# Kernel tuning notes

Hardware: AMD Instinct MI355X
Metric: run time of the kernel (lower is better)

## Reference

```python
import jax, jax.numpy as jnp
import numpy as np
import math

# ---- model dims (match init_kwargs) ----
D_MODEL = 1024
EXPAND = 2
HEADDIM = 64
D_STATE = 128
NGROUPS = 1
CHUNK = 64
A_FLOOR = 1e-4
D_INNER = EXPAND * D_MODEL            # 2048
NHEADS = D_INNER // HEADDIM           # 32
ROPE_DIM = D_STATE // 2               # rope_fraction=0.5 -> rotate half the state dims
NROPE = ROPE_DIM // 2                 # 32 rotation angles
D_IN_PROJ = D_INNER + 2 * D_STATE * NGROUPS + 3 * NHEADS + NROPE  # 2432
B, L = 2, 2048
EPS = 1e-5


def setup_inputs() -> dict:
    key = jax.random.key(0)
    ks = jax.random.split(key, 5)
    u = jax.random.normal(ks[0], (B, L, D_MODEL), dtype=jnp.float32)
    W_in = jax.random.normal(ks[1], (D_IN_PROJ, D_MODEL), dtype=jnp.float32) * 0.02
    W_out = jax.random.normal(ks[2], (D_MODEL, D_INNER), dtype=jnp.float32) * 0.02
    # dt_bias init as in the torch module
    dt_min, dt_max, dt_floor = 1e-3, 1e-1, 1e-4
    dt = jnp.exp(jax.random.uniform(ks[3], (NHEADS,)) * (math.log(dt_max) - math.log(dt_min)) + math.log(dt_min))
    dt = jnp.maximum(dt, dt_floor)
    dt_bias = dt + jnp.log(-jnp.expm1(-dt))
    B_bias = jnp.ones((NHEADS, D_STATE), dtype=jnp.float32)
    C_bias = jnp.ones((NHEADS, D_STATE), dtype=jnp.float32)
    Bnorm_w = jnp.ones((D_STATE,), dtype=jnp.float32)
    Cnorm_w = jnp.ones((D_STATE,), dtype=jnp.float32)
    D = jnp.ones((NHEADS,), dtype=jnp.float32)
    return {"u": u, "W_in": W_in, "dt_bias": dt_bias, "B_bias": B_bias, "C_bias": C_bias,
            "Bnorm_w": Bnorm_w, "Cnorm_w": Cnorm_w, "D": D, "W_out": W_out}


def _rmsnorm(v, w):
    return v * jax.lax.rsqrt(jnp.mean(v * v, axis=-1, keepdims=True) + EPS) * w


def _rope(v, cos, sin):
    # rotate first 2*NROPE dims of last axis (pairs (i, i+NROPE)); rest untouched
    x1 = v[..., :NROPE]
    x2 = v[..., NROPE:2 * NROPE]
    rest = v[..., 2 * NROPE:]
    return jnp.concatenate([x1 * cos - x2 * sin, x1 * sin + x2 * cos, rest], axis=-1)


def _forward(u, W_in, dt_bias, B_bias, C_bias, Bnorm_w, Cnorm_w, D, W_out):
    b, l, _ = u.shape
    proj = jnp.einsum('bld,ed->ble', u, W_in)
    idx = np.cumsum([D_INNER, D_STATE * NGROUPS, D_STATE * NGROUPS, NHEADS, NHEADS, NHEADS])[:-1].tolist()
    x, Braw, Craw, dd_dt, dd_A, trap_angles = jnp.split(proj, [D_INNER, D_INNER + D_STATE, D_INNER + 2 * D_STATE,
                                                                D_INNER + 2 * D_STATE + NHEADS,
                                                                D_INNER + 2 * D_STATE + 2 * NHEADS], axis=-1)
    trap = trap_angles[..., :NHEADS]
    angles = trap_angles[..., NHEADS:NHEADS + NROPE]
    x = x.reshape(b, l, NHEADS, HEADDIM)

    # discretization scalars per (b,l,h)
    A = -jax.nn.softplus(dd_A)
    A = jnp.minimum(A, -A_FLOOR)
    DT = jax.nn.softplus(dd_dt + dt_bias)
    la = A * DT                      # log of per-step decay (negative)
    a = jnp.exp(la)

    # RMSNorm on B/C (ngroups=1), broadcast to heads, add per-head bias
    Bn = _rmsnorm(Braw, Bnorm_w)[:, :, None, :] + B_bias   # (b,l,h,n)
    Cn = _rmsnorm(Craw, Cnorm_w)[:, :, None, :] + C_bias

    # inline RoPE: cumulative angle Theta_t = cumsum(angles_t * dt_t)
    theta = angles[:, :, None, :] * DT[..., None]           # (b,l,h,r)
    Theta = jnp.cumsum(theta, axis=1)
    cosT, sinT = jnp.cos(Theta), jnp.sin(Theta)
    Bn = _rope(Bn, cosT, sinT)
    Cn = _rope(Cn, cosT, sinT)

    # trapezoidal integration weights: dt*(lam*B_t x_t + (1-lam)*exp(A dt)*B_{t-1} x_{t-1})
    lam = jax.nn.sigmoid(trap)
    w1 = DT * lam                    # current-token weight  (b,l,h)
    w2 = DT * (1.0 - lam) * a        # previous-token weight (includes decay)
    Bp = jnp.pad(Bn, ((0, 0), (1, 0), (0, 0), (0, 0)))[:, :-1]
    xp = jnp.pad(x, ((0, 0), (1, 0), (0, 0), (0, 0)))[:, :-1]

    # ---- chunked selective scan ----
    nc = l // CHUNK
    ck = lambda t: t.reshape(b, nc, CHUNK, *t.shape[2:])
    xc, xpc, Bc, Bpc, Cc = ck(x), ck(xp), ck(Bn), ck(Bp), ck(Cn)
    lac, w1c, w2c = ck(la), ck(w1), ck(w2)
    Acum = jnp.cumsum(lac, axis=2)                           # (b,z,t,h)

    mask = jnp.tril(jnp.ones((CHUNK, CHUNK), dtype=u.dtype))
    decay = jnp.exp(Acum[:, :, :, None, :] - Acum[:, :, None, :, :]) * mask[None, None, :, :, None]  # (b,z,t,s,h)

    CB1 = jnp.einsum('bzthn,bzshn->bztsh', Cc, Bc)
    CB2 = jnp.einsum('bzthn,bzshn->bztsh', Cc, Bpc)
    M1 = decay * CB1 * w1c[:, :, None, :, :]
    M2 = decay * CB2 * w2c[:, :, None, :, :]
    Yintra = jnp.einsum('bztsh,bzshp->bzthp', M1, xc) + jnp.einsum('bztsh,bzshp->bzthp', M2, xpc)

    # contribution of each chunk to its end-of-chunk state
    r = jnp.exp(Acum[:, :, -1:, :] - Acum)                   # (b,z,t,h)
    U = (jnp.einsum('bzsh,bzshn,bzshp->bzhpn', r * w1c, Bc, xc)
         + jnp.einsum('bzsh,bzshn,bzshp->bzhpn', r * w2c, Bpc, xpc))
    cd = jnp.exp(Acum[:, :, -1, :])                          # whole-chunk decay (b,z,h)

    def step(h, inp):
        U_, c_ = inp
        return c_[..., None, None] * h + U_, h               # emit state at chunk start
    h0 = jnp.zeros((b, NHEADS, HEADDIM, D_STATE), dtype=u.dtype)
    _, states = jax.lax.scan(step, h0, (jnp.moveaxis(U, 1, 0), jnp.moveaxis(cd, 1, 0)))  # (z,b,h,p,n)

    Ystate = jnp.einsum('bzthn,bzth,zbhpn->bzthp', Cc, jnp.exp(Acum), states)
    y = (Yintra + Ystate).reshape(b, l, NHEADS, HEADDIM) + x * D[None, None, :, None]
    y = y.reshape(b, l, D_INNER)
    return jnp.einsum('bli,oi->blo', y, W_out)


def reference(u, W_in, dt_bias, B_bias, C_bias, Bnorm_w, Cnorm_w, D, W_out):
    return _forward(u, W_in, dt_bias, B_bias, C_bias, Bnorm_w, Cnorm_w, D, W_out)
```

## Files before the change

kernel.cpp:

```cpp
#include <hip/hip_runtime.h>
#include <hip/hip_bf16.h>
#include <math.h>

typedef unsigned short u16;
typedef __attribute__((ext_vector_type(8))) short s16x8;
typedef __attribute__((ext_vector_type(4))) float f32x4;

#define BB 2
#define LL 2048
#define DMODEL 1024
#define DI 2048
#define NH 32
#define HD 64
#define DS 128
#define NR 32
#define CH 64
#define NC 32
#define DIP 2432
#define NTOK (BB*LL)
#define PAW 384
#define CVW 264

__device__ __forceinline__ float bf2f(u16 u){ union{unsigned i; float f;} c; c.i=((unsigned)u)<<16; return c.f; }
__device__ __forceinline__ u16 f2bf(float f){ __hip_bfloat16 h=__float2bfloat16(f); return *reinterpret_cast<u16*>(&h); }
__device__ __forceinline__ float softplusf(float x){ return fmaxf(x,0.f) + log1pf(expf(-fabsf(x))); }

__device__ __forceinline__ void gl_lds16(const void* g, void* l){
  __builtin_amdgcn_global_load_lds((const __attribute__((address_space(1))) void*)g,
                                   (__attribute__((address_space(3))) void*)l, 16, 0, 0);
}

__device__ __forceinline__ s16x8 ldswz(const u16* base, int r, int kunit){
  return *(const s16x8*)&base[r*128 + ((kunit ^ (r&7))<<3)];
}
__device__ __forceinline__ s16x8 ldswz64(const u16* base, int r, int kunit){
  return *(const s16x8*)&base[r*64 + ((kunit ^ (r&7))<<3)];
}
__device__ __forceinline__ float ldswz64_s(const u16* base, int r, int n){
  return bf2f(base[r*64 + (((n>>3) ^ (r&7))<<3) + (n&7)]);
}
__device__ __forceinline__ s16x8 ld72(const u16* base, int r, int kelem){
  return *(const s16x8*)&base[r*72 + kelem];
}

#define CQ1 ((NTOK*DMODEL)/4)
#define CQ2 ((DIP*DMODEL)/4)
#define CQ3 ((DMODEL*DI)/4)
__global__ __launch_bounds__(256) void k_cast3(const float* __restrict__ u, const float* __restrict__ Wi,
                                               const float* __restrict__ Wo,
                                               u16* __restrict__ ub, u16* __restrict__ wib,
                                               u16* __restrict__ wob){
  int i = blockIdx.x*256 + threadIdx.x;
  const float* src; u16* dst; int q;
  if (i < CQ1){ src = u; dst = ub; q = i; }
  else if (i < CQ1+CQ2){ src = Wi; dst = wib; q = i - CQ1; }
  else if (i < CQ1+CQ2+CQ3){ src = Wo; dst = wob; q = i - CQ1 - CQ2; }
  else return;
  float4 v = *(const float4*)&src[(size_t)q*4];
  ushort4 o; o.x=f2bf(v.x); o.y=f2bf(v.y); o.z=f2bf(v.z); o.w=f2bf(v.w);
  *(ushort4*)&dst[(size_t)q*4] = o;
}

__global__ __launch_bounds__(512) void k_gemm_in(const u16* __restrict__ A,
                                                 const u16* __restrict__ Bm,
                                                 float* __restrict__ pAux,
                                                 u16* __restrict__ Xtg){
  __shared__ u16 lA[128*64];
  __shared__ u16 lB[128*64];
  int tid = threadIdx.x;
  int l = tid & 63, w = tid >> 6;
  int nwg = gridDim.x*gridDim.y;
  int flat = blockIdx.y*gridDim.x + blockIdx.x;
  int cpx = nwg >> 3;
  int swz = (flat & 7)*cpx + (flat >> 3);
  int bx = swz % gridDim.x, by = swz / gridDim.x;
  int bm = by*128, bn = bx*128;
  int wr = w >> 2, wc = w & 3;
  const f32x4 vzero = {0.f,0.f,0.f,0.f};
  f32x4 acc[4][2];
  #pragma unroll
  for (int i=0;i<4;i++)
    #pragma unroll
    for (int j=0;j<2;j++) acc[i][j] = vzero;

  for (int kt=0; kt<DMODEL; kt+=64){
    __syncthreads();
    #pragma unroll
    for (int cc=0; cc<2; cc++){
      int s = w*2 + cc;
      int uu = s*64 + l;
      int r = uu >> 3, jl = uu & 7;
      int j = jl ^ (r & 7);
      gl_lds16(A  + (size_t)(bm+r)*DMODEL + kt + j*8, &lA[s*512]);
      gl_lds16(Bm + (size_t)(bn+r)*DMODEL + kt + j*8, &lB[s*512]);
    }
    __syncthreads();
    #pragma unroll
    for (int ks=0; ks<2; ks++){
      s16x8 af[4], bf[2];
      #pragma unroll
      for (int i=0;i<4;i++){
        int row = wr*64 + i*16 + (l&15);
        int j = ks*4 + (l>>4);
        af[i] = *(const s16x8*)&lA[row*64 + (j^(row&7))*8];
      }
      #pragma unroll
      for (int i=0;i<2;i++){
        int row = wc*32 + i*16 + (l&15);
        int j = ks*4 + (l>>4);
        bf[i] = *(const s16x8*)&lB[row*64 + (j^(row&7))*8];
      }
      #pragma unroll
      for (int i=0;i<4;i++)
        #pragma unroll
        for (int jj=0;jj<2;jj++)
          acc[i][jj] = __builtin_amdgcn_mfma_f32_16x16x32_bf16(af[i], bf[jj], acc[i][jj], 0,0,0);
    }
  }
  int col0 = bn + wc*32 + (l&15);
  int row0 = bm + wr*64 + (l>>4)*4;
  if (bn < DI){
    int h = (bn + wc*32) >> 6;
    int pbase = (wc & 1)*32 + (l&15);
    int b = bm >> 11;
    #pragma unroll
    for (int i=0;i<4;i++){
      int lbase = (bm & (LL-1)) + wr*64 + (l>>4)*4 + i*16;
      #pragma unroll
      for (int jj=0;jj<2;jj++){
        int p = pbase + jj*16;
        ushort4 o;
        o.x = f2bf(acc[i][jj][0]); o.y = f2bf(acc[i][jj][1]);
        o.z = f2bf(acc[i][jj][2]); o.w = f2bf(acc[i][jj][3]);
        *(ushort4*)&Xtg[((size_t)(b*NH + h)*HD + p)*LL + lbase] = o;
      }
    }
  } else {
    #pragma unroll
    for (int i=0;i<4;i++)
      #pragma unroll
      for (int jj=0;jj<2;jj++)
        #pragma unroll
        for (int q=0;q<4;q++)
          pAux[(size_t)(row0 + i*16 + q)*PAW + col0 + jj*16 - DI] = acc[i][jj][q];
  }
}

__global__ __launch_bounds__(256) void k_prep(const float* __restrict__ pAux,
                                              const float* __restrict__ dt_bias,
                                              const float* __restrict__ Bnw,
                                              const float* __restrict__ Cnw,
                                              float* __restrict__ Bnr, float* __restrict__ Cnr,
                                              float* __restrict__ DTg, float* __restrict__ lag,
                                              float* __restrict__ w1g, float* __restrict__ w2g){
  int tid = threadIdx.x;
  int r = tid >> 7, t = tid & 127;
  int row = blockIdx.x*2 + r;
  const float* pr = pAux + (size_t)row*PAW;
  float bv = pr[t], cv = pr[128+t];
  float sb = bv*bv, sc = cv*cv;
  for (int o=32;o;o>>=1){ sb += __shfl_down(sb,o); sc += __shfl_down(sc,o); }
  __shared__ float red[8];
  if ((tid&63)==0){ red[(tid>>6)*2]=sb; red[(tid>>6)*2+1]=sc; }
  __syncthreads();
  float ssb = red[r*4]+red[r*4+2], ssc = red[r*4+1]+red[r*4+3];
  float rb = rsqrtf(ssb/DS + 1e-5f), rc = rsqrtf(ssc/DS + 1e-5f);
  Bnr[(size_t)row*DS+t] = bv*rb*Bnw[t];
  Cnr[(size_t)row*DS+t] = cv*rc*Cnw[t];
  if (t < NH){
    int h = t;
    float Av = -softplusf(pr[288+h]); Av = fminf(Av, -1e-4f);
    float DT = softplusf(pr[256+h] + dt_bias[h]);
    float la = Av*DT;
    float lam = 1.f/(1.f+expf(-pr[320+h]));
    DTg[row*NH+h] = DT;
    lag[row*NH+h] = la;
    w1g[row*NH+h] = DT*lam;
    w2g[row*NH+h] = DT*(1.f-lam)*expf(la);
  }
}

__global__ __launch_bounds__(64) void k_theta_part(const float* __restrict__ pAux, const float* __restrict__ DTg,
                                                   float* __restrict__ Spart){
  int blk = blockIdx.x*2 + (threadIdx.x>>5);
  int j = threadIdx.x & 31;
  int h = blk % NH; int z = (blk/NH)%NC; int b = blk/(NH*NC);
  float acc = 0.f;
  for (int i=0;i<CH;i++){
    int row = b*LL + z*CH + i;
    acc += DTg[row*NH+h] * pAux[(size_t)row*PAW + 352 + j];
  }
  Spart[(size_t)blk*NR + j] = acc;
}

__global__ void k_theta_scan(float* __restrict__ Spart){
  int idx = blockIdx.x*blockDim.x + threadIdx.x;
  int j = idx % NR; int h = (idx/NR)%NH; int b = idx/(NR*NH);
  float acc = 0.f;
  for (int z=0;z<NC;z++){
    size_t o = (size_t)((b*NC+z)*NH + h)*NR + j;
    float t = Spart[o]; Spart[o] = acc; acc += t;
  }
}

__global__ __launch_bounds__(256) void k_acum(const float* __restrict__ lag,
                                              const float* __restrict__ w1g,
                                              const float* __restrict__ w2g,
                                              float* __restrict__ CV,
                                              float* __restrict__ Acumg,
                                              float* __restrict__ cdg){
  int blk = blockIdx.x*4 + (threadIdx.x>>6);
  int l = threadIdx.x & 63;
  int h = blk & 31, z = (blk>>5)&31, b = blk>>10;
  int row = b*LL + z*CH + l;
  float la = lag[row*NH+h], w1 = w1g[row*NH+h], w2 = w2g[row*NH+h];
  float a = la;
  #pragma unroll
  for (int o=1;o<64;o<<=1){ float t = __shfl_up(a,o); a += (l>=o) ? t : 0.f; }
  float Acm = __shfl(a, 31);
  float Alast = __shfl(a, 63);
  float eA = expf(a - Acm);
  float emA = expf(Acm - a);
  float rfac = expf(Alast - a);
  float rw1 = rfac*w1, rw2 = rfac*w2;
  float rw1p = __shfl_up(rw1, 1);
  float* cv = CV + (size_t)blk*CVW;
  cv[l] = eA;
  cv[64 + l] = emA*w1;
  cv[128 + l] = emA*w2;
  cv[192 + l] = (l>0 ? rw1p : 0.f) + rw2;
  if (l == 63){ cv[192+64] = rw1; cdg[blk] = expf(Alast); }
  Acumg[(size_t)blk*CH + l] = a;
}

__global__ __launch_bounds__(256) void k_rope2(const float* __restrict__ Bnr,
                                               const float* __restrict__ Cnr,
                                               const float* __restrict__ pAux,
                                               const float* __restrict__ DTg,
                                               const float* __restrict__ Spart,
                                               const float* __restrict__ B_bias,
                                               const float* __restrict__ C_bias,
                                               u16* __restrict__ Bn, u16* __restrict__ Cn){
  __shared__ float thS[64][33];
  int blk = blockIdx.x; int h = blk&31, z=(blk>>5)&31, b=blk>>10;
  int l0 = z*CH; int tid = threadIdx.x;
  int l = tid & 63, w = tid >> 6;
  {
    int row = b*LL + l0 + l;
    float dt = DTg[row*NH + h];
    int j0 = w*8;
    float4 a0 = *(const float4*)&pAux[(size_t)row*PAW + 352 + j0];
    float4 a1 = *(const float4*)&pAux[(size_t)row*PAW + 352 + j0 + 4];
    float v[8] = {dt*a0.x, dt*a0.y, dt*a0.z, dt*a0.w, dt*a1.x, dt*a1.y, dt*a1.z, dt*a1.w};
    #pragma unroll
    for (int e=0;e<8;e++){
      float s = v[e];
      #pragma unroll
      for (int o=1;o<64;o<<=1){ float t = __shfl_up(s,o); s += (l>=o) ? t : 0.f; }
      thS[l][j0+e] = s + Spart[(size_t)blk*NR + j0 + e];
    }
  }
  __syncthreads();
  const float* bb = B_bias + h*DS;
  const float* cb = C_bias + h*DS;
  #pragma unroll
  for (int it=0; it<8; it++){
    int idx = it*256 + tid;
    int r = idx>>5, j = idx&31;
    int row = b*LL + l0 + r;
    const float* br = Bnr + (size_t)row*DS;
    const float* cr = Cnr + (size_t)row*DS;
    float th = thS[r][j];
    float cs = cosf(th), sn = sinf(th);
    float b0 = br[j]    + bb[j];
    float b1 = br[j+32] + bb[j+32];
    float b2 = br[j+64] + bb[j+64];
    float b3 = br[j+96] + bb[j+96];
    float c0 = cr[j]    + cb[j];
    float c1 = cr[j+32] + cb[j+32];
    float c2 = cr[j+64] + cb[j+64];
    float c3 = cr[j+96] + cb[j+96];
    float obA = b0*cs - b1*sn, obB = b0*sn + b1*cs;
    float ocA = c0*cs - c1*sn, ocB = c0*sn + c1*cs;
    u16* bnp = Bn + ((size_t)row*NH + h)*DS;
    u16* cnp = Cn + ((size_t)row*NH + h)*DS;
    bnp[j]    = f2bf(obA); bnp[j+32] = f2bf(obB);
    bnp[j+64] = f2bf(b2);  bnp[j+96] = f2bf(b3);
    cnp[j]    = f2bf(ocA); cnp[j+32] = f2bf(ocB);
    cnp[j+64] = f2bf(c2);  cnp[j+96] = f2bf(c3);
  }
}

__global__ __launch_bounds__(512) void k_chunk_a(
    const u16* __restrict__ Xtg, const u16* __restrict__ Bn,
    const u16* __restrict__ Cn,
    const float* __restrict__ CV, const float* __restrict__ Dgl,
    u16* __restrict__ Yb, u16* __restrict__ Ugb){
  __shared__ u16 BsBT[65*128];
  __shared__ u16 CsMc[64*128];
  __shared__ u16 Xt64[64*64];
  __shared__ u16 Bp[128], Xp[64];
  __shared__ float cvS[260];
  __shared__ float mc0s[64];
  int blk = blockIdx.x;
  int h = blk&31, z=(blk>>5)&31, b=blk>>10;
  int l0 = z*CH;
  int tid = threadIdx.x; int l = tid&63, w = tid>>6;
  int wA = w >> 1, wB = w & 1;
  size_t bh = (size_t)(b*NH + h);

  if (tid < 128){
    u16 v = 0;
    if (z > 0) v = Bn[((size_t)(b*LL+l0-1)*NH + h)*DS + tid];
    BsBT[tid] = v; Bp[tid] = v;
  } else if (tid < 192){
    int p = tid - 128;
    u16 v = 0;
    if (z > 0) v = Xtg[(bh*HD + p)*LL + l0 - 1];
    Xp[p] = v;
  }
  if (tid < 257) cvS[tid] = CV[(size_t)blk*CVW + tid];
  #pragma unroll
  for (int cc=0; cc<2; cc++){
    int c = w*2 + cc;
    { int r = 1 + 4*c + (l>>4);
      gl_lds16(Bn + ((size_t)(b*LL+l0+r-1)*NH+h)*DS + (((l&15)^(r&7))<<3), &BsBT[(1+4*c)*128]); }
    { int r = 4*c + (l>>4);
      gl_lds16(Cn + ((size_t)(b*LL+l0+r)*NH+h)*DS + (((l&15)^(r&7))<<3), &CsMc[4*c*128]); }
  }
  {
    int uu = w*64 + l; int r = uu>>3, jl = uu&7, j = jl^(r&7);
    gl_lds16(Xtg + (bh*HD + r)*LL + l0 + j*8, &Xt64[w*512]);
  }
  __syncthreads();

  const f32x4 vzero = {0.f,0.f,0.f,0.f};
  f32x4 acb[2];
  #pragma unroll
  for (int j=0;j<2;j++) acb[j] = vzero;
  #pragma unroll
  for (int ks=0; ks<4; ks++){
    s16x8 af = ldswz(CsMc, 16*wA + (l&15), ks*4 + (l>>4));
    #pragma unroll
    for (int j=0;j<2;j++){
      s16x8 bfr = ldswz(BsBT, 1 + 16*(wB*2+j) + (l&15), ks*4 + (l>>4));
      acb[j] = __builtin_amdgcn_mfma_f32_16x16x32_bf16(af, bfr, acb[j], 0,0,0);
    }
  }
  {
    int t = tid>>3, part = tid&7;
    float s = 0.f;
    #pragma unroll
    for (int uu=0; uu<2; uu++){
      int u = part*2 + uu;
      s16x8 cr = *(const s16x8*)&CsMc[t*128 + ((u^(t&7))<<3)];
      s16x8 br = *(const s16x8*)&BsBT[u<<3];
      #pragma unroll
      for (int e=0;e<8;e++) s += bf2f(cr[e])*bf2f(br[e]);
    }
    s += __shfl_xor(s, 1); s += __shfl_xor(s, 2); s += __shfl_xor(s, 4);
    if (part == 0) mc0s[t] = s * cvS[t] * cvS[128];
  }
  __syncthreads();

  u16 tv[16];
  #pragma unroll
  for (int it=0; it<16; it++){
    int i = it*512 + tid;
    int n = i & 127, k = i >> 7;
    int r = k + 1;
    tv[it] = BsBT[r*128 + ((((n>>3) ^ (r&7))<<3) | (n&7))];
  }
  #pragma unroll
  for (int j=0;j<2;j++){
    #pragma unroll
    for (int q=0;q<4;q++){
      int t = 16*wA + (l>>4)*4 + q;
      int k = 16*(wB*2+j) + (l&15);
      int sp = k + 1;
      float g = 0.f;
      if (sp <= t+1) g += cvS[63+sp];
      if (sp <= t)   g += cvS[128+sp];
      g *= cvS[t];
      CsMc[t*72 + k] = f2bf(acb[j][q] * g);
    }
  }
  __syncthreads();

  #pragma unroll
  for (int it=0; it<16; it++){
    int i = it*512 + tid;
    int n = i & 127, k = i >> 7;
    float v = bf2f(tv[it]) * cvS[192 + k + 1];
    BsBT[n*64 + ((((k>>3) ^ (n&7))<<3) | (k&7))] = f2bf(v);
  }
  __syncthreads();

  f32x4 ay[2];
  #pragma unroll
  for (int j=0;j<2;j++) ay[j] = vzero;
  #pragma unroll
  for (int ks=0; ks<2; ks++){
    s16x8 af = ld72(CsMc, 16*wA + (l&15), ks*32 + (l>>4)*8);
    #pragma unroll
    for (int j=0;j<2;j++){
      s16x8 bfr = ldswz64(Xt64, 16*(wB*2+j) + (l&15), ks*4 + (l>>4));
      ay[j] = __builtin_amdgcn_mfma_f32_16x16x32_bf16(af, bfr, ay[j], 0,0,0);
    }
  }
  {
    float Dh = Dgl[h];
    #pragma unroll
    for (int j=0;j<2;j++){
      #pragma unroll
      for (int q=0;q<4;q++){
        int t = 16*wA + (l>>4)*4 + q;
        int p = 16*(wB*2+j) + (l&15);
        float xval = ldswz64_s(Xt64, p, t);
        float yv = ay[j][q] + mc0s[t]*bf2f(Xp[p]) + Dh*xval;
        Yb[((size_t)(b*LL + l0 + t))*DI + h*HD + p] = f2bf(yv);
      }
    }
  }

  f32x4 au[4];
  #pragma unroll
  for (int j=0;j<4;j++) au[j] = vzero;
  #pragma unroll
  for (int ks=0; ks<2; ks++){
    s16x8 af = ldswz64(Xt64, 16*wA + (l&15), ks*4 + (l>>4));
    #pragma unroll
    for (int j=0;j<4;j++){
      s16x8 bfr = ldswz64(BsBT, 16*(wB*4+j) + (l&15), ks*4 + (l>>4));
      au[j] = __builtin_amdgcn_mfma_f32_16x16x32_bf16(af, bfr, au[j], 0,0,0);
    }
  }
  {
    float vw0 = cvS[192];
    #pragma unroll
    for (int j=0;j<4;j++){
      #pragma unroll
      for (int q=0;q<4;q++){
        int p = 16*wA + (l>>4)*4 + q;
        int n = 16*(wB*4+j) + (l&15);
        float uv = au[j][q] + vw0*bf2f(Xp[p])*bf2f(Bp[n]);
        Ugb[(size_t)blk*(HD*DS) + p*DS + n] = f2bf(uv);
      }
    }
  }
}

__global__ __launch_bounds__(256) void k_scan(u16* __restrict__ Ugb, const float* __restrict__ cdg){
  int idx = blockIdx.x*256 + threadIdx.x;
  int pn8 = (idx & 1023)*8;
  int h  = (idx >> 10) & 31;
  int b  = idx >> 15;
  float hs[8];
  #pragma unroll
  for (int e=0;e<8;e++) hs[e] = 0.f;
  for (int z=0;z<NC;z++){
    size_t o = ((size_t)((b*NC+z)*NH) + h)*(HD*DS) + pn8;
    s16x8 v = *(s16x8*)&Ugb[o];
    float cd = cdg[(b*NC+z)*NH + h];
    s16x8 wv;
    #pragma unroll
    for (int e=0;e<8;e++){
      float tmp = bf2f((u16)v[e]);
      wv[e] = (short)f2bf(hs[e]);
      hs[e] = cd*hs[e] + tmp;
    }
    *(s16x8*)&Ugb[o] = wv;
  }
}

__global__ __launch_bounds__(512) void k_state(
    const u16* __restrict__ Cn, const u16* __restrict__ Ugb,
    const float* __restrict__ Acumg, u16* __restrict__ Yb){
  __shared__ u16 Cs[64*128];
  __shared__ u16 Sb[64*128];
  __shared__ float eAs[64];
  int blk = blockIdx.x;
  int h = blk & 31, z = (blk>>5)&31, b = blk>>10;
  int l0 = z*CH;
  int tid = threadIdx.x;
  int l = tid & 63, w = tid >> 6;
  int wA = w >> 1, wB = w & 1;

  if (tid < 64) eAs[tid] = expf(Acumg[(size_t)blk*CH + tid]);
  #pragma unroll
  for (int cc=0; cc<2; cc++){
    int c = w*2 + cc;
    int r = 4*c + (l>>4);
    gl_lds16(Cn + ((size_t)(b*LL + l0 + r)*NH + h)*DS + (((l&15)^(r&7))<<3), &Cs[4*c*128]);
    gl_lds16(Ugb + (size_t)blk*(HD*DS) + (size_t)r*DS + (((l&15)^(r&7))<<3), &Sb[4*c*128]);
  }
  __syncthreads();

  f32x4 as[2];
  const f32x4 vzero = {0.f,0.f,0.f,0.f};
  #pragma unroll
  for (int j=0;j<2;j++) as[j] = vzero;
  #pragma unroll
  for (int ks=0; ks<4; ks++){
    s16x8 af = ldswz(Cs, 16*wA + (l&15), ks*4 + (l>>4));
    #pragma unroll
    for (int j=0;j<2;j++){
      s16x8 bfr = ldswz(Sb, 16*(wB*2+j) + (l&15), ks*4 + (l>>4));
      as[j] = __builtin_amdgcn_mfma_f32_16x16x32_bf16(af, bfr, as[j], 0,0,0);
    }
  }
  #pragma unroll
  for (int j=0;j<2;j++){
    #pragma unroll
    for (int q=0;q<4;q++){
      int t = 16*wA + (l>>4)*4 + q;
      int p = 16*(wB*2+j) + (l&15);
      size_t idx = ((size_t)(b*LL + l0 + t))*DI + h*HD + p;
      Yb[idx] = f2bf(bf2f(Yb[idx]) + eAs[t]*as[j][q]);
    }
  }
}

template<int N, int K>
__global__ __launch_bounds__(512) void k_mfma_nt64(const u16* __restrict__ A,
                                                   const u16* __restrict__ Bm,
                                                   float* __restrict__ C){
  __shared__ u16 lA[128*64];
  __shared__ u16 lB[64*64];
  int tid = threadIdx.x;
  int l = tid & 63, w = tid >> 6;
  int nwg = gridDim.x*gridDim.y;
  int flat = blockIdx.y*gridDim.x + blockIdx.x;
  int cpx = nwg >> 3;
  int swz = (flat & 7)*cpx + (flat >> 3);
  int bx = swz % gridDim.x, by = swz / gridDim.x;
  int bm = by*128, bn = bx*64;
  int wr = w >> 1, wc = w & 1;
  const f32x4 vzero = {0.f,0.f,0.f,0.f};
  f32x4 acc[2][2];
  #pragma unroll
  for (int i=0;i<2;i++)
    #pragma unroll
    for (int j=0;j<2;j++) acc[i][j] = vzero;

  for (int kt=0; kt<K; kt+=64){
    __syncthreads();
    #pragma unroll
    for (int cc=0; cc<2; cc++){
      int s = w*2 + cc;
      int uu = s*64 + l;
      int r = uu >> 3, jl = uu & 7;
      int j = jl ^ (r & 7);
      gl_lds16(A + (size_t)(bm+r)*K + kt + j*8, &lA[s*512]);
    }
    {
      int uu = w*64 + l;
      int r = uu >> 3, jl = uu & 7;
      int j = jl ^ (r & 7);
      gl_lds16(Bm + (size_t)(bn+r)*K + kt + j*8, &lB[w*512]);
    }
    __syncthreads();
    #pragma unroll
    for (int ks=0; ks<2; ks++){
      s16x8 af[2], bf[2];
      #pragma unroll
      for (int i=0;i<2;i++){
        int row = wr*32 + i*16 + (l&15);
        int j = ks*4 + (l>>4);
        af[i] = *(const s16x8*)&lA[row*64 + (j^(row&7))*8];
      }
      #pragma unroll
      for (int i=0;i<2;i++){
        int row = wc*32 + i*16 + (l&15);
        int j = ks*4 + (l>>4);
        bf[i] = *(const s16x8*)&lB[row*64 + (j^(row&7))*8];
      }
      #pragma unroll
      for (int i=0;i<2;i++)
        #pragma unroll
        for (int jj=0;jj<2;jj++)
          acc[i][jj] = __builtin_amdgcn_mfma_f32_16x16x32_bf16(af[i], bf[jj], acc[i][jj], 0,0,0);
    }
  }
  int col0 = bn + wc*32 + (l&15);
  int row0 = bm + wr*32 + (l>>4)*4;
  #pragma unroll
  for (int i=0;i<2;i++)
    #pragma unroll
    for (int jj=0;jj<2;jj++)
      #pragma unroll
      for (int q=0;q<4;q++)
        C[(size_t)(row0 + i*16 + q)*N + col0 + jj*16] = acc[i][jj][q];
}

constexpr size_t OFF_PAUX  = 0;
constexpr size_t OFF_XTG   = 6291456;
constexpr size_t OFF_BNR   = 23068672;
constexpr size_t OFF_CNR   = 25165824;
constexpr size_t OFF_DT    = 27262976;
constexpr size_t OFF_LA    = 27787264;
constexpr size_t OFF_W1    = 28311552;
constexpr size_t OFF_W2    = 28835840;
constexpr size_t OFF_SPART = 29360128;
constexpr size_t OFF_CV    = 29622272;
constexpr size_t OFF_ACUM  = 31784960;
constexpr size_t OFF_CD    = 32309248;
constexpr size_t OFF_Y     = 32317440;
constexpr size_t OFF_BN    = 49094656;
constexpr size_t OFF_CN    = 82649088;
constexpr size_t OFF_R1    = 149757952;
constexpr size_t OFF_UBF   = OFF_R1;
constexpr size_t OFF_WINBF = OFF_R1 + 16777216;
constexpr size_t OFF_UGB   = OFF_R1;
constexpr size_t OFF_WOUTBF= 183312384;

extern "C" void kernel_launch(void* const* d_in, const int* in_sizes, int n_in,
                              void* d_out, int out_size, void* d_ws, size_t ws_size,
                              hipStream_t stream) {
  const float* u       = (const float*)d_in[0];
  const float* W_in    = (const float*)d_in[1];
  const float* dt_bias = (const float*)d_in[2];
  const float* B_bias  = (const float*)d_in[3];
  const float* C_bias  = (const float*)d_in[4];
  const float* Bnw     = (const float*)d_in[5];
  const float* Cnw     = (const float*)d_in[6];
  const float* Dg      = (const float*)d_in[7];
  const float* W_out   = (const float*)d_in[8];
  float* out = (float*)d_out;
  char* ws = (char*)d_ws;

  float* pAux  = (float*)(ws + OFF_PAUX);
  u16*   Xtg   = (u16*)  (ws + OFF_XTG);
  float* Bnr   = (float*)(ws + OFF_BNR);
  float* Cnr   = (float*)(ws + OFF_CNR);
  float* DTg   = (float*)(ws + OFF_DT);
  float* lag   = (float*)(ws + OFF_LA);
  float* w1g   = (float*)(ws + OFF_W1);
  float* w2g   = (float*)(ws + OFF_W2);
  float* Spart = (float*)(ws + OFF_SPART);
  float* CVp   = (float*)(ws + OFF_CV);
  float* Acumg = (float*)(ws + OFF_ACUM);
  float* cdg   = (float*)(ws + OFF_CD);
  u16*   Yb    = (u16*)  (ws + OFF_Y);
  u16*   Bn    = (u16*)  (ws + OFF_BN);
  u16*   Cn    = (u16*)  (ws + OFF_CN);
  u16*   u_bf  = (u16*)  (ws + OFF_UBF);
  u16*   Win_bf= (u16*)  (ws + OFF_WINBF);
  u16*   Ugb   = (u16*)  (ws + OFF_UGB);
  u16*   Wout_bf=(u16*)  (ws + OFF_WOUTBF);

  k_cast3<<<(CQ1+CQ2+CQ3+255)/256, 256, 0, stream>>>(u, W_in, W_out, u_bf, Win_bf, Wout_bf);
  k_gemm_in<<<dim3(DIP/128, NTOK/128), 512, 0, stream>>>(u_bf, Win_bf, pAux, Xtg);

  k_prep      <<<NTOK/2, 256, 0, stream>>>(pAux, dt_bias, Bnw, Cnw, Bnr, Cnr, DTg, lag, w1g, w2g);
  k_theta_part<<<(BB*NC*NH)/2, 64, 0, stream>>>(pAux, DTg, Spart);
  k_theta_scan<<<(BB*NH*NR)/256, 256, 0, stream>>>(Spart);
  k_acum      <<<(BB*NC*NH)/4, 256, 0, stream>>>(lag, w1g, w2g, CVp, Acumg, cdg);
  k_rope2     <<<BB*NC*NH, 256, 0, stream>>>(Bnr, Cnr, pAux, DTg, Spart, B_bias, C_bias, Bn, Cn);

  k_chunk_a<<<BB*NC*NH, 512, 0, stream>>>(Xtg, Bn, Cn, CVp, Dg, Yb, Ugb);
  k_scan   <<<(BB*NH*HD*DS)/(256*8), 256, 0, stream>>>(Ugb, cdg);
  k_state  <<<BB*NC*NH, 512, 0, stream>>>(Cn, Ugb, Acumg, Yb);

  k_mfma_nt64<DMODEL, DI><<<dim3(DMODEL/64, NTOK/128), 512, 0, stream>>>(Yb, Wout_bf, out);

  (void)in_sizes; (void)n_in; (void)out_size; (void)ws_size;
}
```

Baseline: 166.9 us.

## Fuse theta partial sums into k_acum, remap blocks across XCDs, shrink scan blocks

Removes the separate k_theta_part kernel by computing the per-chunk dt-weighted angle sums inside k_acum through a shared-memory transpose and reduction. This saves one launch and a second strided read of pAux. k_rope2, k_chunk_a and k_state now remap blockIdx so that consecutive logical blocks land on the same one of 8 XCDs, which should improve L2 locality. k_scan uses 128-thread blocks to spread its work over more blocks. The costs are extra LDS use in k_acum and an added __syncthreads.

```diff
diff --git a/kernel.cpp b/kernel.cpp
--- a/kernel.cpp
+++ b/kernel.cpp
@@ -180,19 +180,6 @@
   }
 }
 
-__global__ __launch_bounds__(64) void k_theta_part(const float* __restrict__ pAux, const float* __restrict__ DTg,
-                                                   float* __restrict__ Spart){
-  int blk = blockIdx.x*2 + (threadIdx.x>>5);
-  int j = threadIdx.x & 31;
-  int h = blk % NH; int z = (blk/NH)%NC; int b = blk/(NH*NC);
-  float acc = 0.f;
-  for (int i=0;i<CH;i++){
-    int row = b*LL + z*CH + i;
-    acc += DTg[row*NH+h] * pAux[(size_t)row*PAW + 352 + j];
-  }
-  Spart[(size_t)blk*NR + j] = acc;
-}
-
 __global__ void k_theta_scan(float* __restrict__ Spart){
   int idx = blockIdx.x*blockDim.x + threadIdx.x;
   int j = idx % NR; int h = (idx/NR)%NH; int b = idx/(NR*NH);
@@ -206,10 +193,15 @@
 __global__ __launch_bounds__(256) void k_acum(const float* __restrict__ lag,
                                               const float* __restrict__ w1g,
                                               const float* __restrict__ w2g,
+                                              const float* __restrict__ pAux,
+                                              const float* __restrict__ DTg,
                                               float* __restrict__ CV,
                                               float* __restrict__ Acumg,
-                                              float* __restrict__ cdg){
-  int blk = blockIdx.x*4 + (threadIdx.x>>6);
+                                              float* __restrict__ cdg,
+                                              float* __restrict__ Spart){
+  __shared__ float thS[4][64][33];
+  int wv = threadIdx.x >> 6;
+  int blk = blockIdx.x*4 + wv;
   int l = threadIdx.x & 63;
   int h = blk & 31, z = (blk>>5)&31, b = blk>>10;
   int row = b*LL + z*CH + l;
@@ -231,6 +223,28 @@
   cv[192 + l] = (l>0 ? rw1p : 0.f) + rw2;
   if (l == 63){ cv[192+64] = rw1; cdg[blk] = expf(Alast); }
   Acumg[(size_t)blk*CH + l] = a;
+
+  {
+    float dt = DTg[row*NH + h];
+    const float* ap = pAux + (size_t)row*PAW + 352;
+    #pragma unroll
+    for (int e4=0; e4<8; e4++){
+      float4 a4 = *(const float4*)&ap[e4*4];
+      thS[wv][l][e4*4+0] = dt*a4.x;
+      thS[wv][l][e4*4+1] = dt*a4.y;
+      thS[wv][l][e4*4+2] = dt*a4.z;
+      thS[wv][l][e4*4+3] = dt*a4.w;
+    }
+  }
+  __syncthreads();
+  {
+    int j = l & 31, r0 = (l>>5)*32;
+    float s = 0.f;
+    #pragma unroll
+    for (int r=0;r<32;r++) s += thS[wv][r0+r][j];
+    s += __shfl_xor(s, 32);
+    if (l < 32) Spart[(size_t)blk*NR + j] = s;
+  }
 }
 
 __global__ __launch_bounds__(256) void k_rope2(const float* __restrict__ Bnr,
@@ -242,7 +256,9 @@
                                                const float* __restrict__ C_bias,
                                                u16* __restrict__ Bn, u16* __restrict__ Cn){
   __shared__ float thS[64][33];
-  int blk = blockIdx.x; int h = blk&31, z=(blk>>5)&31, b=blk>>10;
+  int cpx = gridDim.x >> 3;
+  int blk = (blockIdx.x & 7)*cpx + (blockIdx.x >> 3);
+  int h = blk&31, z=(blk>>5)&31, b=blk>>10;
   int l0 = z*CH; int tid = threadIdx.x;
   int l = tid & 63, w = tid >> 6;
   {
@@ -302,7 +318,8 @@
   __shared__ u16 Bp[128], Xp[64];
   __shared__ float cvS[260];
   __shared__ float mc0s[64];
-  int blk = blockIdx.x;
+  int cpx = gridDim.x >> 3;
+  int blk = (blockIdx.x & 7)*cpx + (blockIdx.x >> 3);
   int h = blk&31, z=(blk>>5)&31, b=blk>>10;
   int l0 = z*CH;
   int tid = threadIdx.x; int l = tid&63, w = tid>>6;
@@ -450,8 +467,8 @@
   }
 }
 
-__global__ __launch_bounds__(256) void k_scan(u16* __restrict__ Ugb, const float* __restrict__ cdg){
-  int idx = blockIdx.x*256 + threadIdx.x;
+__global__ __launch_bounds__(128) void k_scan(u16* __restrict__ Ugb, const float* __restrict__ cdg){
+  int idx = blockIdx.x*128 + threadIdx.x;
   int pn8 = (idx & 1023)*8;
   int h  = (idx >> 10) & 31;
   int b  = idx >> 15;
@@ -479,7 +496,8 @@
   __shared__ u16 Cs[64*128];
   __shared__ u16 Sb[64*128];
   __shared__ float eAs[64];
-  int blk = blockIdx.x;
+  int cpx = gridDim.x >> 3;
+  int blk = (blockIdx.x & 7)*cpx + (blockIdx.x >> 3);
   int h = blk & 31, z = (blk>>5)&31, b = blk>>10;
   int l0 = z*CH;
   int tid = threadIdx.x;
@@ -653,13 +671,12 @@
   k_gemm_in<<<dim3(DIP/128, NTOK/128), 512, 0, stream>>>(u_bf, Win_bf, pAux, Xtg);
 
   k_prep      <<<NTOK/2, 256, 0, stream>>>(pAux, dt_bias, Bnw, Cnw, Bnr, Cnr, DTg, lag, w1g, w2g);
-  k_theta_part<<<(BB*NC*NH)/2, 64, 0, stream>>>(pAux, DTg, Spart);
+  k_acum      <<<(BB*NC*NH)/4, 256, 0, stream>>>(lag, w1g, w2g, pAux, DTg, CVp, Acumg, cdg, Spart);
   k_theta_scan<<<(BB*NH*NR)/256, 256, 0, stream>>>(Spart);
-  k_acum      <<<(BB*NC*NH)/4, 256, 0, stream>>>(lag, w1g, w2g, CVp, Acumg, cdg);
   k_rope2     <<<BB*NC*NH, 256, 0, stream>>>(Bnr, Cnr, pAux, DTg, Spart, B_bias, C_bias, Bn, Cn);
 
   k_chunk_a<<<BB*NC*NH, 512, 0, stream>>>(Xtg, Bn, Cn, CVp, Dg, Yb, Ugb);
-  k_scan   <<<(BB*NH*HD*DS)/(256*8), 256, 0, stream>>>(Ugb, cdg);
+  k_scan   <<<(BB*NH*HD*DS)/(128*8), 128, 0, stream>>>(Ugb, cdg);
   k_state  <<<BB*NC*NH, 512, 0, stream>>>(Cn, Ugb, Acumg, Yb);
 
   k_mfma_nt64<DMODEL, DI><<<dim3(DMODEL/64, NTOK/128), 512, 0, stream>>>(Yb, Wout_bf, out);
```

Result: faster. 161.0 us (-3.6%).
